# Kernel tuning notes

Hardware: AMD Instinct MI355X
Metric: run time of the kernel (lower is better)

Reference implementation:

```python
import jax, jax.numpy as jnp
import numpy as np

N, S, W, H = 256, 64, 256, 32   # node_num, sensor_num, slide_win, gru_hid_size
ALPHA = 0.2
NEG = -9e15


def gat(h, adj, Wm, a):
    """pyGAT GraphAttentionLayer (concat=False, dropout=0 / eval).
    h: [..., M, din], adj: [..., M, M], Wm: [..., din, dout], a: [..., 2*dout]."""
    Wh = jnp.einsum('...mi,...io->...mo', h, Wm)
    dout = Wm.shape[-1]
    f1 = jnp.einsum('...mo,...o->...m', Wh, a[..., :dout])
    f2 = jnp.einsum('...mo,...o->...m', Wh, a[..., dout:])
    e = jax.nn.leaky_relu(f1[..., :, None] + f2[..., None, :], negative_slope=ALPHA)
    att = jax.nn.softmax(jnp.where(adj > 0, e, NEG), axis=-1)
    return jnp.einsum('...mk,...ko->...mo', att, Wh)


def gru_cell(h, x, Wih, Whh, bih, bhh):
    # per-node batched torch GRU cell; gate order r, z, n
    gi = jnp.einsum('ngi,ni->ng', Wih, x) + bih
    gh = jnp.einsum('ngh,nh->ng', Whh, h) + bhh
    ir, iz, inn = jnp.split(gi, 3, axis=-1)
    hr, hz, hn = jnp.split(gh, 3, axis=-1)
    r = jax.nn.sigmoid(ir + hr)
    z = jax.nn.sigmoid(iz + hz)
    n = jnp.tanh(inn + r * hn)
    return (1.0 - z) * n + z * h


def gru2(xseq, h0, Wih0, Whh0, bih0, bhh0, Wih1, Whh1, bih1, bhh1):
    # xseq: [N, S, Din] (seq axis = sensor axis), h0: [2, N, H] -> ([N,S,H], [2,N,H])
    def step(carry, x_t):
        h0c, h1c = carry
        h0n = gru_cell(h0c, x_t, Wih0, Whh0, bih0, bhh0)
        h1n = gru_cell(h1c, h0n, Wih1, Whh1, bih1, bhh1)
        return (h0n, h1n), h1n
    (h0f, h1f), ys = jax.lax.scan(step, (h0[0], h0[1]), jnp.swapaxes(xseq, 0, 1))
    return jnp.swapaxes(ys, 0, 1), jnp.stack([h0f, h1f])


def setup_inputs():
    key = jax.random.key(0)
    ks = jax.random.split(key, 32)
    def rn(k, shape, scale=0.05):
        return jax.random.normal(k, shape, dtype=jnp.float32) * scale
    inp = {}
    inp['x'] = jax.random.normal(ks[0], (N, S, W), dtype=jnp.float32)
    inp['Feature_adj_sub'] = jax.random.randint(ks[1], (N, S, S), 0, 2).astype(jnp.float32)
    inp['Time_adj_sub'] = jax.random.randint(ks[2], (N, W, W), 0, 2).astype(jnp.float32)
    inp['adj'] = jax.random.randint(ks[3], (N, N), 0, 2).astype(jnp.float32)
    inp['H_pre'] = jax.random.normal(ks[4], (2, N, H), dtype=jnp.float32)
    # per-node GAT params (stacked over nodes)
    inp['Fatt_W'] = rn(ks[5], (N, W, W)); inp['Fatt_a'] = rn(ks[6], (N, 2 * W))
    inp['Tatt_W'] = rn(ks[7], (N, S, S)); inp['Tatt_a'] = rn(ks[8], (N, 2 * S))
    # per-node 2-layer GRU params
    inp['Wih0'] = rn(ks[9], (N, 3 * H, 3 * W)); inp['Whh0'] = rn(ks[10], (N, 3 * H, H))
    inp['bih0'] = rn(ks[11], (N, 3 * H)); inp['bhh0'] = rn(ks[12], (N, 3 * H))
    inp['Wih1'] = rn(ks[13], (N, 3 * H, H)); inp['Whh1'] = rn(ks[14], (N, 3 * H, H))
    inp['bih1'] = rn(ks[15], (N, 3 * H)); inp['bhh1'] = rn(ks[16], (N, 3 * H))
    # per-node 3-layer FC
    inp['fc1_w'] = rn(ks[17], (N, H, H)); inp['fc1_b'] = rn(ks[18], (N, H))
    inp['fc2_w'] = rn(ks[19], (N, H, H)); inp['fc2_b'] = rn(ks[20], (N, H))
    inp['fc3_w'] = rn(ks[21], (N, 1, H)); inp['fc3_b'] = rn(ks[22], (N, 1))
    # global output GATs
    inp['oW'] = rn(ks[23], (S, S)); inp['oa'] = rn(ks[24], (2 * S,))
    inp['o1W'] = rn(ks[25], (S, S)); inp['o1a'] = rn(ks[26], (2 * S,))
    inp['o2W'] = rn(ks[27], (2 * S, S)); inp['o2a'] = rn(ks[28], (2 * S,))
    return inp


def reference(x, Feature_adj_sub, Time_adj_sub, adj, H_pre,
              Fatt_W, Fatt_a, Tatt_W, Tatt_a,
              Wih0, Whh0, bih0, bhh0, Wih1, Whh1, bih1, bhh1,
              fc1_w, fc1_b, fc2_w, fc2_b, fc3_w, fc3_b,
              oW, oa, o1W, o1a, o2W, o2a):
    # batched over all nodes at once (replaces Python loop over node_num)
    Fat = gat(x, Feature_adj_sub, Fatt_W, Fatt_a)                    # [N,S,W]
    Tat = gat(jnp.swapaxes(x, 1, 2), Time_adj_sub, Tatt_W, Tatt_a)   # [N,W,S]
    cat_at = jnp.concatenate([Fat, jnp.swapaxes(Tat, 1, 2), x], axis=-1)  # [N,S,3W]
    gru_out, cat_H = gru2(cat_at, H_pre, Wih0, Whh0, bih0, bhh0,
                          Wih1, Whh1, bih1, bhh1)                    # [N,S,H],[2,N,H]
    h = jax.nn.relu(jnp.einsum('nsh,nkh->nsk', gru_out, fc1_w) + fc1_b[:, None, :])
    h = jax.nn.relu(jnp.einsum('nsh,nkh->nsk', h, fc2_w) + fc2_b[:, None, :])
    ct = (jnp.einsum('nsh,nkh->nsk', h, fc3_w) + fc3_b[:, None, :])[..., 0]  # [N,S]
    out = gat(ct, adj, oW, oa)
    out1 = gat(ct, adj, o1W, o1a)
    finalout = gat(jnp.concatenate([out, out1], axis=-1), adj, o2W, o2a)
    return finalout, cat_H
```

## Files before the change

### kernel.cpp

```cpp
#include <hip/hip_runtime.h>
#include <hip/hip_bf16.h>

__device__ __forceinline__ float sigf(float x){ return __builtin_amdgcn_rcpf(1.f+__expf(-x)); }
__device__ __forceinline__ float tanhfa(float x){
  return 1.f - 2.f*__builtin_amdgcn_rcpf(1.f + __expf(2.f*x));
}

#define ALPHA 0.2f
#define NEGV  -9e15f


__device__ __forceinline__ void gl2lds16(const float* g, float* l){
  __builtin_amdgcn_global_load_lds(
      (const __attribute__((address_space(1))) void*)g,
      (__attribute__((address_space(3))) void*)l, 16, 0, 0);
}

__global__ __launch_bounds__(256) void k_mask(const float* __restrict__ src,
                                              unsigned* __restrict__ dst, int nelem){
  const int stride = gridDim.x * blockDim.x;
  const int lane = threadIdx.x & 63;
  for (int e = blockIdx.x*blockDim.x + threadIdx.x; e < nelem; e += stride){
    unsigned long long m = __ballot(src[e] > 0.f);
    if (lane == 0)       dst[e >> 5] = (unsigned)m;
    else if (lane == 32) dst[e >> 5] = (unsigned)(m >> 32);
  }
}

__global__ __launch_bounds__(256) void k3_wht(const float* __restrict__ x,
                                              const float* __restrict__ TW,
                                              const float* __restrict__ Ta,
                                              float* __restrict__ WhTt,
                                              float* __restrict__ Tf1p,
                                              float* __restrict__ Tf2p){
  const int n = blockIdx.x >> 1, ch = blockIdx.x & 1, c0 = ch*32;
  const int tid = threadIdx.x;
  __shared__ float Wm[64][36];
  __shared__ float as1[32], as2[32];
  for (int idx = tid; idx < 2048; idx += 256){
    int k = idx >> 5, cc = idx & 31;
    Wm[k][cc] = TW[n*4096 + k*64 + c0 + cc];
  }
  if (tid < 32){ as1[tid] = Ta[n*128 + c0 + tid]; as2[tid] = Ta[n*128 + 64 + c0 + tid]; }
  __syncthreads();
  const int i = tid;
  const float* xn = x + n*16384;
  float acc[32];
#pragma unroll
  for (int c = 0; c < 32; ++c) acc[c] = 0.f;
#pragma unroll 2
  for (int k = 0; k < 64; ++k){
    float xv = xn[k*256 + i];
    const float* wr = &Wm[k][0];
#pragma unroll
    for (int c = 0; c < 32; ++c) acc[c] = fmaf(xv, wr[c], acc[c]);
  }
  float f1 = 0.f, f2 = 0.f;
#pragma unroll
  for (int c = 0; c < 32; ++c){ f1 = fmaf(acc[c], as1[c], f1); f2 = fmaf(acc[c], as2[c], f2); }
  Tf1p[ch*65536 + n*256 + i] = f1;
  Tf2p[ch*65536 + n*256 + i] = f2;
  float* o = WhTt + n*16384 + i*64 + c0;
#pragma unroll
  for (int q = 0; q < 8; ++q)
    *(float4*)&o[4*q] = make_float4(acc[4*q], acc[4*q+1], acc[4*q+2], acc[4*q+3]);
}

__global__ __launch_bounds__(256) void k4_tat(const float* __restrict__ WhTt,
                                              const float* __restrict__ Tf1p,
                                              const float* __restrict__ Tf2p,
                                              const unsigned* __restrict__ maskT,
                                              float* __restrict__ TatT){
  const int n = blockIdx.x >> 1, ch = blockIdx.x & 1, c0 = ch*32;
  const int tid = threadIdx.x;
  __shared__ float wtL[8192];
  __shared__ float ptb[8192];
  __shared__ float f2s[256];
  __shared__ float ssum[256];
  __shared__ float wmax[4];
  {
    const int w = tid >> 6, l = tid & 63;
    const float* src = WhTt + n*16384 + (w*64 + (l>>3))*64 + c0 + (l&7)*4;
    float* dst = &wtL[w*2048];
#pragma unroll
    for (int r = 0; r < 8; ++r) gl2lds16(src + r*512, dst + r*256);
  }
  const float f1  = Tf1p[n*256 + tid] + Tf1p[65536 + n*256 + tid];
  const float f2v = Tf2p[n*256 + tid] + Tf2p[65536 + n*256 + tid];
  f2s[tid] = f2v;
  unsigned mw[8];
#pragma unroll
  for (int w = 0; w < 8; ++w) mw[w] = maskT[n*2048 + tid*8 + w];
  float wm = f2v;
#pragma unroll
  for (int d = 1; d < 64; d <<= 1) wm = fmaxf(wm, __shfl_xor(wm, d));
  if ((tid & 63) == 0) wmax[tid >> 6] = wm;
  asm volatile("s_waitcnt vmcnt(0)" ::: "memory");
  __syncthreads();
  const float mb = fmaxf(fmaxf(wmax[0], wmax[1]), fmaxf(wmax[2], wmax[3]));
  const float tm = f1 + mb;
  const float m  = (tm > 0.f) ? tm : ALPHA*tm;
  const int iq = tid & 63, cq = tid >> 6;
  float acc[4][8];
#pragma unroll
  for (int r = 0; r < 4; ++r)
#pragma unroll
    for (int c = 0; c < 8; ++c) acc[r][c] = 0.f;
  float sloc = 0.f;
  for (int jt = 0; jt < 8; ++jt){
    const int j0 = jt*32;
#pragma unroll
    for (int jj = 0; jj < 32; jj += 4){
      const float4 f2q = *(const float4*)&f2s[j0 + jj];
      const unsigned mk = mw[(j0 + jj) >> 5];
      const int sh = (j0 + jj) & 31;
      float t0 = f1 + f2q.x; t0 = (t0 > 0.f) ? t0 : ALPHA*t0;
      float t1 = f1 + f2q.y; t1 = (t1 > 0.f) ? t1 : ALPHA*t1;
      float t2 = f1 + f2q.z; t2 = (t2 > 0.f) ? t2 : ALPHA*t2;
      float t3 = f1 + f2q.w; t3 = (t3 > 0.f) ? t3 : ALPHA*t3;
      const float e0 = ((mk >> (sh+0)) & 1u) ? __expf(t0 - m) : 0.f;
      const float e1 = ((mk >> (sh+1)) & 1u) ? __expf(t1 - m) : 0.f;
      const float e2 = ((mk >> (sh+2)) & 1u) ? __expf(t2 - m) : 0.f;
      const float e3 = ((mk >> (sh+3)) & 1u) ? __expf(t3 - m) : 0.f;
      sloc += (e0 + e1) + (e2 + e3);
      ptb[(jj+0)*256 + tid] = e0;
      ptb[(jj+1)*256 + tid] = e1;
      ptb[(jj+2)*256 + tid] = e2;
      ptb[(jj+3)*256 + tid] = e3;
    }
    __syncthreads();
#pragma unroll 4
    for (int jj = 0; jj < 32; ++jj){
      const float4 p4 = *(const float4*)&ptb[jj*256 + 4*iq];
      const float4 w0 = *(const float4*)&wtL[(j0+jj)*32 + cq*8];
      const float4 w1 = *(const float4*)&wtL[(j0+jj)*32 + cq*8 + 4];
#pragma unroll
      for (int r = 0; r < 4; ++r){
        const float pv = (r == 0) ? p4.x : (r == 1) ? p4.y : (r == 2) ? p4.z : p4.w;
        acc[r][0] = fmaf(pv, w0.x, acc[r][0]);
        acc[r][1] = fmaf(pv, w0.y, acc[r][1]);
        acc[r][2] = fmaf(pv, w0.z, acc[r][2]);
        acc[r][3] = fmaf(pv, w0.w, acc[r][3]);
        acc[r][4] = fmaf(pv, w1.x, acc[r][4]);
        acc[r][5] = fmaf(pv, w1.y, acc[r][5]);
        acc[r][6] = fmaf(pv, w1.z, acc[r][6]);
        acc[r][7] = fmaf(pv, w1.w, acc[r][7]);
      }
    }
    __syncthreads();
  }
  ssum[tid] = sloc;
  __syncthreads();
  float* o = TatT + n*16384;
#pragma unroll
  for (int r = 0; r < 4; ++r){
    const int i2 = 4*iq + r;
    const float sv = ssum[i2];
    const float inv = (sv > 0.f) ? __builtin_amdgcn_rcpf(sv) : 0.f;
#pragma unroll
    for (int cc = 0; cc < 8; ++cc)
      o[(c0 + cq*8 + cc)*256 + i2] = acc[r][cc] * inv;
  }
}

__global__ __launch_bounds__(256) void k1_whf(const float* __restrict__ x,
                                              const float* __restrict__ FW,
                                              float* __restrict__ WhF){
  const int n = blockIdx.x >> 1, ch = blockIdx.x & 1, c0 = ch*128;
  const int tid = threadIdx.x;
  __shared__ float xt[16384];
  {
    const int w = tid >> 6, l = tid & 63;
    const float* xg = x + n*16384 + w*4096 + l*4;
    float* ld = &xt[w*4096];
#pragma unroll
    for (int j = 0; j < 16; ++j) gl2lds16(xg + j*256, ld + j*256);
  }
  asm volatile("s_waitcnt vmcnt(0)" ::: "memory");
  __syncthreads();
  const int cq = tid & 31, iq = tid >> 5;
  const int cc = c0 + cq*4;
  const float* Wn = FW + (size_t)n*65536 + cc;
  const float* xrow = &xt[iq*8*256];
  float acc[8][4];
#pragma unroll
  for (int i = 0; i < 8; ++i)
#pragma unroll
    for (int c = 0; c < 4; ++c) acc[i][c] = 0.f;
#pragma unroll 2
  for (int k4 = 0; k4 < 64; ++k4){
    const float4 w0 = *(const float4*)&Wn[(4*k4+0)*256];
    const float4 w1 = *(const float4*)&Wn[(4*k4+1)*256];
    const float4 w2 = *(const float4*)&Wn[(4*k4+2)*256];
    const float4 w3 = *(const float4*)&Wn[(4*k4+3)*256];
#pragma unroll
    for (int i = 0; i < 8; ++i){
      const float4 xv = *(const float4*)&xrow[i*256 + 4*k4];
      acc[i][0] = fmaf(xv.x, w0.x, acc[i][0]); acc[i][0] = fmaf(xv.y, w1.x, acc[i][0]);
      acc[i][0] = fmaf(xv.z, w2.x, acc[i][0]); acc[i][0] = fmaf(xv.w, w3.x, acc[i][0]);
      acc[i][1] = fmaf(xv.x, w0.y, acc[i][1]); acc[i][1] = fmaf(xv.y, w1.y, acc[i][1]);
      acc[i][1] = fmaf(xv.z, w2.y, acc[i][1]); acc[i][1] = fmaf(xv.w, w3.y, acc[i][1]);
      acc[i][2] = fmaf(xv.x, w0.z, acc[i][2]); acc[i][2] = fmaf(xv.y, w1.z, acc[i][2]);
      acc[i][2] = fmaf(xv.z, w2.z, acc[i][2]); acc[i][2] = fmaf(xv.w, w3.z, acc[i][2]);
      acc[i][3] = fmaf(xv.x, w0.w, acc[i][3]); acc[i][3] = fmaf(xv.y, w1.w, acc[i][3]);
      acc[i][3] = fmaf(xv.z, w2.w, acc[i][3]); acc[i][3] = fmaf(xv.w, w3.w, acc[i][3]);
    }
  }
  float* o = WhF + n*16384 + cc;
#pragma unroll
  for (int i = 0; i < 8; ++i)
    *(float4*)&o[(iq*8 + i)*256] = make_float4(acc[i][0], acc[i][1], acc[i][2], acc[i][3]);
}

__global__ __launch_bounds__(512) void k2_fat(const float* __restrict__ WhF,
                                              const float* __restrict__ Fa,
                                              const float* __restrict__ Fadj,
                                              float* __restrict__ Fat){
  const int n = blockIdx.x, tid = threadIdx.x;
  __shared__ float attT[64][68];
  __shared__ float f1s[64], f2s[64];
  __shared__ float part[64][8][2];
  const float* Wh = WhF + n*16384;
  {
    int i = tid >> 3, q = tid & 7;
    const float* an = Fa + n*512;
    float p1 = 0.f, p2 = 0.f;
    for (int cc = 0; cc < 32; ++cc){
      int c2 = q*32 + cc;
      float w = Wh[i*256 + c2];
      p1 = fmaf(w, an[c2], p1);
      p2 = fmaf(w, an[256 + c2], p2);
    }
    part[i][q][0] = p1; part[i][q][1] = p2;
  }
  __syncthreads();
  if (tid < 64){
    float s1 = 0.f, s2 = 0.f;
#pragma unroll
    for (int q = 0; q < 8; ++q){ s1 += part[tid][q][0]; s2 += part[tid][q][1]; }
    f1s[tid] = s1; f2s[tid] = s2;
  }
  __syncthreads();
  if (tid < 64){
    const int r = tid;
    const float f1 = f1s[r];
    const float* adjr = Fadj + n*4096 + r*64;
    unsigned m0 = 0, m1 = 0;
#pragma unroll
    for (int j = 0; j < 32; ++j) if (adjr[j] > 0.f) m0 |= (1u << j);
#pragma unroll
    for (int j = 0; j < 32; ++j) if (adjr[32+j] > 0.f) m1 |= (1u << j);
    float m = -INFINITY;
#pragma unroll
    for (int j = 0; j < 64; ++j){
      float e = f1 + f2s[j]; e = (e > 0.f) ? e : ALPHA*e;
      unsigned bit = (j < 32) ? ((m0 >> j) & 1u) : ((m1 >> (j-32)) & 1u);
      e = bit ? e : NEGV;
      m = fmaxf(m, e);
    }
    float s = 0.f;
#pragma unroll
    for (int j = 0; j < 64; ++j){
      float e = f1 + f2s[j]; e = (e > 0.f) ? e : ALPHA*e;
      unsigned bit = (j < 32) ? ((m0 >> j) & 1u) : ((m1 >> (j-32)) & 1u);
      e = bit ? e : NEGV;
      s += __expf(e - m);
    }
    const float inv = 1.f / s;
#pragma unroll
    for (int j = 0; j < 64; ++j){
      float e = f1 + f2s[j]; e = (e > 0.f) ? e : ALPHA*e;
      unsigned bit = (j < 32) ? ((m0 >> j) & 1u) : ((m1 >> (j-32)) & 1u);
      e = bit ? e : NEGV;
      attT[j][r] = __expf(e - m) * inv;
    }
  }
  __syncthreads();
  const int c = tid & 255, ih = tid >> 8;
  float acc[32];
#pragma unroll
  for (int i = 0; i < 32; ++i) acc[i] = 0.f;
#pragma unroll 2
  for (int j = 0; j < 64; ++j){
    float w = Wh[j*256 + c];
    const float* ar = &attT[j][ih*32];
#pragma unroll
    for (int i = 0; i < 32; ++i) acc[i] = fmaf(ar[i], w, acc[i]);
  }
  float* o = Fat + n*16384;
#pragma unroll
  for (int i = 0; i < 32; ++i) o[(ih*32 + i)*256 + c] = acc[i];
}

__global__ __launch_bounds__(256) void k5_gi0(const float* __restrict__ Fat,
                                              const float* __restrict__ TatT,
                                              const float* __restrict__ x,
                                              const float* __restrict__ Wih0,
                                              float* __restrict__ P0,
                                              float* __restrict__ P1,
                                              float* __restrict__ P2){
  const int n = blockIdx.x & 255, s = blockIdx.x >> 8;
  const int tid = threadIdx.x;
  const int a = tid & 31, b = tid >> 5;
  __shared__ float cl[2][2304];
  const float* src = (s == 0) ? (Fat + n*16384)
                   : (s == 1) ? (TatT + n*16384)
                              : (x + n*16384);
  const float* Wseg = Wih0 + (size_t)n*73728 + s*256 + (size_t)b*12*768;
  const int tr = tid >> 2, kq = tid & 3;
  const float* cg = src + tr*256 + kq*8;
  const int cwo = tr*36 + kq*8;
  {
    float4 ra = *(const float4*)cg;
    float4 rb = *(const float4*)(cg + 4);
    *(float4*)&cl[0][cwo]     = ra;
    *(float4*)&cl[0][cwo + 4] = rb;
  }
  __syncthreads();
  float acc[12][2];
#pragma unroll
  for (int gi = 0; gi < 12; ++gi){ acc[gi][0] = 0.f; acc[gi][1] = 0.f; }
#pragma unroll 1
  for (int kt = 0; kt < 8; ++kt){
    const int buf = kt & 1;
    float4 na, nb;
    if (kt < 7){
      na = *(const float4*)(cg + (kt+1)*32);
      nb = *(const float4*)(cg + (kt+1)*32 + 4);
    }
    const float* Wk = Wseg + kt*32;
    const float* c0p = &cl[buf][a*36];
    const float* c1p = &cl[buf][(a+32)*36];
#pragma unroll
    for (int k4 = 0; k4 < 8; ++k4){
      float4 wv[12];
#pragma unroll
      for (int gi = 0; gi < 12; ++gi)
        wv[gi] = *(const float4*)(Wk + (size_t)gi*768 + k4*4);
      const float4 c0 = *(const float4*)(c0p + k4*4);
      const float4 c1 = *(const float4*)(c1p + k4*4);
#pragma unroll
      for (int gi = 0; gi < 12; ++gi){
        float a0 = acc[gi][0], a1 = acc[gi][1];
        a0 = fmaf(wv[gi].x, c0.x, a0); a1 = fmaf(wv[gi].x, c1.x, a1);
        a0 = fmaf(wv[gi].y, c0.y, a0); a1 = fmaf(wv[gi].y, c1.y, a1);
        a0 = fmaf(wv[gi].z, c0.z, a0); a1 = fmaf(wv[gi].z, c1.z, a1);
        a0 = fmaf(wv[gi].w, c0.w, a0); a1 = fmaf(wv[gi].w, c1.w, a1);
        acc[gi][0] = a0; acc[gi][1] = a1;
      }
    }
    if (kt < 7){
      *(float4*)&cl[buf^1][cwo]     = na;
      *(float4*)&cl[buf^1][cwo + 4] = nb;
    }
    __syncthreads();
  }
  float* o = (s == 0) ? (P0 + n*16384)
           : (s == 1) ? (P1 + n*16384)
                      : (P2 + n*8192);
#pragma unroll
  for (int q = 0; q < 3; ++q){
    *(float4*)&o[a*96 + b*12 + q*4] =
        make_float4(acc[4*q][0], acc[4*q+1][0], acc[4*q+2][0], acc[4*q+3][0]);
    *(float4*)&o[(a+32)*96 + b*12 + q*4] =
        make_float4(acc[4*q][1], acc[4*q+1][1], acc[4*q+2][1], acc[4*q+3][1]);
  }
}

__global__ __launch_bounds__(128) void k6_gru(const float* __restrict__ G0,
                                              const float* __restrict__ G1,
                                              const float* __restrict__ G2,
                                              const float* __restrict__ Hpre,
                                              const float* __restrict__ Whh0,
                                              const float* __restrict__ bih0,
                                              const float* __restrict__ bhh0,
                                              const float* __restrict__ Wih1,
                                              const float* __restrict__ Whh1,
                                              const float* __restrict__ bih1,
                                              const float* __restrict__ bhh1,
                                              const float* __restrict__ fc1w,
                                              const float* __restrict__ fc1b,
                                              const float* __restrict__ fc2w,
                                              const float* __restrict__ fc2b,
                                              const float* __restrict__ fc3w,
                                              const float* __restrict__ fc3b,
                                              float* __restrict__ ct,
                                              float* __restrict__ dout){
  const int n = blockIdx.x, tid = threadIdx.x;
  const int wid = tid >> 6, l = tid & 63;
  const int g2 = l & 31, co = (l >> 5) * 16;
  __shared__ float ginS[6144];
  __shared__ float h0buf[2][32];
  __shared__ float h1buf[2][32];
  __shared__ float hist[64][33];
  __shared__ float Wst[32][33];
  __shared__ float b1s[32], b2s[32], w3s[32];
  {
    const float4* p0 = (const float4*)(G0 + n*16384);
    const float4* p1 = (const float4*)(G1 + n*16384);
    const float4* p2 = (const float4*)(G2 + n*8192);
    float4* gs = (float4*)ginS;
#pragma unroll
    for (int j = 0; j < 12; ++j){
      int idx = j*128 + tid;
      float4 a = p0[idx], b = p1[idx], c = p2[idx];
      gs[idx] = make_float4(a.x+b.x+c.x, a.y+b.y+c.y, a.z+b.z+c.z, a.w+b.w+c.w);
    }
  }
  if (tid < 32){
    b1s[tid] = fc1b[n*32 + tid];
    b2s[tid] = fc2b[n*32 + tid];
    w3s[tid] = fc3w[n*32 + tid];
  }
  for (int idx = tid; idx < 1024; idx += 128) Wst[idx>>5][idx&31] = fc1w[n*1024 + idx];
  float wr_[16], wz_[16], wn_[16];
  float ur_[16], uz_[16], un_[16];
  {
    const float* WA = (wid == 0) ? (Whh0 + n*3072) : (Wih1 + n*3072);
#pragma unroll
    for (int q = 0; q < 4; ++q){
      float4 v;
      v = *(const float4*)(WA + g2*32 + co + 4*q);       wr_[4*q]=v.x; wr_[4*q+1]=v.y; wr_[4*q+2]=v.z; wr_[4*q+3]=v.w;
      v = *(const float4*)(WA + (32+g2)*32 + co + 4*q);  wz_[4*q]=v.x; wz_[4*q+1]=v.y; wz_[4*q+2]=v.z; wz_[4*q+3]=v.w;
      v = *(const float4*)(WA + (64+g2)*32 + co + 4*q);  wn_[4*q]=v.x; wn_[4*q+1]=v.y; wn_[4*q+2]=v.z; wn_[4*q+3]=v.w;
    }
    if (wid == 1){
      const float* WB = Whh1 + n*3072;
#pragma unroll
      for (int q = 0; q < 4; ++q){
        float4 v;
        v = *(const float4*)(WB + g2*32 + co + 4*q);       ur_[4*q]=v.x; ur_[4*q+1]=v.y; ur_[4*q+2]=v.z; ur_[4*q+3]=v.w;
        v = *(const float4*)(WB + (32+g2)*32 + co + 4*q);  uz_[4*q]=v.x; uz_[4*q+1]=v.y; uz_[4*q+2]=v.z; uz_[4*q+3]=v.w;
        v = *(const float4*)(WB + (64+g2)*32 + co + 4*q);  un_[4*q]=v.x; un_[4*q+1]=v.y; un_[4*q+2]=v.z; un_[4*q+3]=v.w;
      }
    }
  }
  const float* bip = (wid == 0) ? bih0 : bih1;
  const float* bhp = (wid == 0) ? bhh0 : bhh1;
  const float br = bip[n*96 + g2], bz = bip[n*96 + 32 + g2], bn = bip[n*96 + 64 + g2];
  const float cr = bhp[n*96 + g2], cz = bhp[n*96 + 32 + g2], cn = bhp[n*96 + 64 + g2];
  const float* hp = (wid == 0) ? (Hpre + n*32) : (Hpre + 8192 + n*32);
  float hown = hp[g2];
  float hs[16];
#pragma unroll
  for (int q = 0; q < 4; ++q){
    float4 v = *(const float4*)&hp[co + 4*q];
    hs[4*q]=v.x; hs[4*q+1]=v.y; hs[4*q+2]=v.z; hs[4*q+3]=v.w;
  }
  for (int s = 0; s < 65; ++s){
    __syncthreads();
    if (wid == 0){
      if (s < 64){
        const float gr = ginS[s*96 + g2], gz = ginS[s*96 + 32 + g2], gn = ginS[s*96 + 64 + g2];
        if (s > 0){
#pragma unroll
          for (int q = 0; q < 4; ++q){
            float4 v = *(const float4*)&h0buf[(s-1)&1][co + 4*q];
            hs[4*q]=v.x; hs[4*q+1]=v.y; hs[4*q+2]=v.z; hs[4*q+3]=v.w;
          }
        }
        float pr = 0.f, pz = 0.f, pn = 0.f;
#pragma unroll
        for (int j = 0; j < 16; ++j){
          pr = fmaf(wr_[j], hs[j], pr);
          pz = fmaf(wz_[j], hs[j], pz);
          pn = fmaf(wn_[j], hs[j], pn);
        }
        pr += __shfl_xor(pr, 32);
        pz += __shfl_xor(pz, 32);
        pn += __shfl_xor(pn, 32);
        const float r = sigf(gr + br + pr + cr);
        const float z = sigf(gz + bz + pz + cz);
        const float nn = tanhfa(gn + bn + r*(pn + cn));
        hown = (1.f - z)*nn + z*hown;
        if (l < 32) h0buf[s & 1][g2] = hown;
      }
    } else {
      if (s >= 1){
        const int t = s - 1;
        if (s > 1){
#pragma unroll
          for (int q = 0; q < 4; ++q){
            float4 v = *(const float4*)&h1buf[(s-1)&1][co + 4*q];
            hs[4*q]=v.x; hs[4*q+1]=v.y; hs[4*q+2]=v.z; hs[4*q+3]=v.w;
          }
        }
        float hx[16];
#pragma unroll
        for (int q = 0; q < 4; ++q){
          float4 v = *(const float4*)&h0buf[(s-1)&1][co + 4*q];
          hx[4*q]=v.x; hx[4*q+1]=v.y; hx[4*q+2]=v.z; hx[4*q+3]=v.w;
        }
        float qr = 0.f, qz = 0.f, qn = 0.f, sr = 0.f, sz = 0.f, sn = 0.f;
#pragma unroll
        for (int j = 0; j < 16; ++j){
          qr = fmaf(wr_[j], hx[j], qr);  sr = fmaf(ur_[j], hs[j], sr);
          qz = fmaf(wz_[j], hx[j], qz);  sz = fmaf(uz_[j], hs[j], sz);
          qn = fmaf(wn_[j], hx[j], qn);  sn = fmaf(un_[j], hs[j], sn);
        }
        float vr = qr + sr; vr += __shfl_xor(vr, 32);
        float vz = qz + sz; vz += __shfl_xor(vz, 32);
        qn += __shfl_xor(qn, 32);
        sn += __shfl_xor(sn, 32);
        const float r1 = sigf(vr + br + cr);
        const float z1 = sigf(vz + bz + cz);
        const float n1 = tanhfa(qn + bn + r1*(sn + cn));
        hown = (1.f - z1)*n1 + z1*hown;
        if (l < 32){ h1buf[s & 1][g2] = hown; hist[t][g2] = hown; }
      }
    }
  }
  if (wid == 0 && l < 32) dout[16384 + n*32 + g2] = hown;
  if (wid == 1 && l < 32) dout[16384 + 8192 + n*32 + g2] = hown;
  __syncthreads();
  float r1a[32];
  if (tid < 64){
    float hr[32];
#pragma unroll
    for (int k = 0; k < 32; ++k) hr[k] = hist[tid][k];
#pragma unroll
    for (int k = 0; k < 32; ++k){
      float a0=0.f,a1=0.f,a2=0.f,a3=0.f;
#pragma unroll
      for (int q = 0; q < 32; q += 4){
        a0 = fmaf(hr[q],   Wst[k][q],   a0);
        a1 = fmaf(hr[q+1], Wst[k][q+1], a1);
        a2 = fmaf(hr[q+2], Wst[k][q+2], a2);
        a3 = fmaf(hr[q+3], Wst[k][q+3], a3);
      }
      float v = b1s[k] + ((a0+a1)+(a2+a3));
      r1a[k] = v > 0.f ? v : 0.f;
    }
  }
  __syncthreads();
  for (int idx = tid; idx < 1024; idx += 128) Wst[idx>>5][idx&31] = fc2w[n*1024 + idx];
  __syncthreads();
  if (tid < 64){
    float r2a[32];
#pragma unroll
    for (int k = 0; k < 32; ++k){
      float a0=0.f,a1=0.f,a2=0.f,a3=0.f;
#pragma unroll
      for (int q = 0; q < 32; q += 4){
        a0 = fmaf(r1a[q],   Wst[k][q],   a0);
        a1 = fmaf(r1a[q+1], Wst[k][q+1], a1);
        a2 = fmaf(r1a[q+2], Wst[k][q+2], a2);
        a3 = fmaf(r1a[q+3], Wst[k][q+3], a3);
      }
      float v = b2s[k] + ((a0+a1)+(a2+a3));
      r2a[k] = v > 0.f ? v : 0.f;
    }
    float v = fc3b[n];
#pragma unroll
    for (int k = 0; k < 32; ++k) v = fmaf(r2a[k], w3s[k], v);
    ct[n*64 + tid] = v;
  }
}

__global__ __launch_bounds__(256) void k8a(const float* __restrict__ ct,
                                           const float* __restrict__ W0,
                                           const float* __restrict__ a0,
                                           const float* __restrict__ W1,
                                           const float* __restrict__ a1,
                                           float* __restrict__ WhABt,
                                           float* __restrict__ OF1,
                                           float* __restrict__ OF2){
  const int gat = blockIdx.x >> 2, rq = blockIdx.x & 3, r0 = rq*64;
  const int tid = threadIdx.x;
  const int ii = tid & 63, cq = tid >> 6;
  __shared__ float ctl[64][65];
  __shared__ float Wl[64][68];
  __shared__ float a1s[64], a2s[64];
  __shared__ float red[64][4][2];
  const float* W = gat ? W1 : W0;
  const float* aa = gat ? a1 : a0;
  for (int idx = tid; idx < 4096; idx += 256){
    int i2 = idx >> 6, k = idx & 63;
    ctl[i2][k] = ct[(r0 + i2)*64 + k];
  }
  for (int idx = tid; idx < 4096; idx += 256){
    int k = idx >> 6, c = idx & 63;
    Wl[k][c] = W[k*64 + c];
  }
  if (tid < 64){ a1s[tid] = aa[tid]; a2s[tid] = aa[64 + tid]; }
  __syncthreads();
  float acc[16];
#pragma unroll
  for (int c = 0; c < 16; ++c) acc[c] = 0.f;
#pragma unroll 2
  for (int k = 0; k < 64; ++k){
    float v = ctl[ii][k];
    const float* wr = &Wl[k][cq*16];
#pragma unroll
    for (int c = 0; c < 16; ++c) acc[c] = fmaf(v, wr[c], acc[c]);
  }
  float p1 = 0.f, p2 = 0.f;
#pragma unroll
  for (int c = 0; c < 16; ++c){
    p1 = fmaf(acc[c], a1s[cq*16 + c], p1);
    p2 = fmaf(acc[c], a2s[cq*16 + c], p2);
  }
  red[ii][cq][0] = p1; red[ii][cq][1] = p2;
  float* o = WhABt + gat*16384;
#pragma unroll
  for (int c = 0; c < 16; ++c) o[(cq*16 + c)*256 + r0 + ii] = acc[c];
  __syncthreads();
  if (cq == 0){
    OF1[gat*256 + r0 + ii] = red[ii][0][0] + red[ii][1][0] + red[ii][2][0] + red[ii][3][0];
    OF2[gat*256 + r0 + ii] = red[ii][0][1] + red[ii][1][1] + red[ii][2][1] + red[ii][3][1];
  }
}

__global__ __launch_bounds__(256) void k8b(const float* __restrict__ WhABt,
                                           const float* __restrict__ OF1,
                                           const float* __restrict__ OF2,
                                           const unsigned* __restrict__ maskA,
                                           float* __restrict__ OUTT){
  const int gat = blockIdx.x >> 2, c0 = (blockIdx.x & 3) * 16;
  const int i = threadIdx.x;
  __shared__ float wt[4096];
  __shared__ float f2s[256];
  __shared__ float wmax[4];
  {
    const int w = i >> 6, l = i & 63;
    const float* src = WhABt + gat*16384 + c0*256 + w*1024 + l*4;
    float* dst = &wt[w*1024];
#pragma unroll
    for (int r = 0; r < 4; ++r) gl2lds16(src + r*256, dst + r*256);
  }
  const float f1  = OF1[gat*256 + i];
  const float f2v = OF2[gat*256 + i];
  f2s[i] = f2v;
  unsigned mw[8];
#pragma unroll
  for (int w = 0; w < 8; ++w) mw[w] = maskA[i*8 + w];
  float wm = f2v;
#pragma unroll
  for (int d = 1; d < 64; d <<= 1) wm = fmaxf(wm, __shfl_xor(wm, d));
  if ((i & 63) == 0) wmax[i >> 6] = wm;
  asm volatile("s_waitcnt vmcnt(0)" ::: "memory");
  __syncthreads();
  const float mb = fmaxf(fmaxf(wmax[0], wmax[1]), fmaxf(wmax[2], wmax[3]));
  const float tm = f1 + mb;
  const float m  = (tm > 0.f) ? tm : ALPHA*tm;
  float acc[16];
#pragma unroll
  for (int c = 0; c < 16; ++c) acc[c] = 0.f;
  float s = 0.f;
#pragma unroll 2
  for (int jb = 0; jb < 64; ++jb){
    const float4 f2q = *(const float4*)&f2s[jb*4];
    const unsigned mk = mw[jb >> 3];
    const int sh = (jb & 7) * 4;
    float t0 = f1 + f2q.x; t0 = (t0 > 0.f) ? t0 : ALPHA*t0;
    float t1 = f1 + f2q.y; t1 = (t1 > 0.f) ? t1 : ALPHA*t1;
    float t2 = f1 + f2q.z; t2 = (t2 > 0.f) ? t2 : ALPHA*t2;
    float t3 = f1 + f2q.w; t3 = (t3 > 0.f) ? t3 : ALPHA*t3;
    const float e0 = ((mk >> (sh+0)) & 1u) ? __expf(t0 - m) : 0.f;
    const float e1 = ((mk >> (sh+1)) & 1u) ? __expf(t1 - m) : 0.f;
    const float e2 = ((mk >> (sh+2)) & 1u) ? __expf(t2 - m) : 0.f;
    const float e3 = ((mk >> (sh+3)) & 1u) ? __expf(t3 - m) : 0.f;
    s += (e0 + e1) + (e2 + e3);
#pragma unroll
    for (int c = 0; c < 16; ++c){
      const float4 wv = *(const float4*)&wt[c*256 + jb*4];
      acc[c] = fmaf(e0, wv.x, fmaf(e1, wv.y, fmaf(e2, wv.z, fmaf(e3, wv.w, acc[c]))));
    }
  }
  const float inv = (s > 0.f) ? __builtin_amdgcn_rcpf(s) : 0.f;
#pragma unroll
  for (int c = 0; c < 16; ++c) OUTT[gat*16384 + (c0+c)*256 + i] = acc[c] * inv;
}

__global__ __launch_bounds__(256) void k8c(const float* __restrict__ OUTT,
                                           const float* __restrict__ W2,
                                           const float* __restrict__ a2,
                                           float* __restrict__ Wh2,
                                           float* __restrict__ F1B,
                                           float* __restrict__ F2B){
  const int r0 = blockIdx.x * 32;
  const int tid = threadIdx.x;
  const int ii = tid & 31, cq = tid >> 5;
  __shared__ float W2l[128][68];
  __shared__ float a1s[64], a2s[64];
  __shared__ float red[32][8][2];
  for (int idx = tid; idx < 8192; idx += 256){
    int k = idx >> 6, c = idx & 63;
    W2l[k][c] = W2[k*64 + c];
  }
  if (tid < 64){ a1s[tid] = a2[tid]; a2s[tid] = a2[64 + tid]; }
  __syncthreads();
  float acc[8];
#pragma unroll
  for (int c = 0; c < 8; ++c) acc[c] = 0.f;
#pragma unroll 2
  for (int k = 0; k < 128; ++k){
    float v = OUTT[(k >> 6)*16384 + (k & 63)*256 + r0 + ii];
    const float* wr = &W2l[k][cq*8];
#pragma unroll
    for (int c = 0; c < 8; ++c) acc[c] = fmaf(v, wr[c], acc[c]);
  }
  float p1 = 0.f, p2 = 0.f;
#pragma unroll
  for (int c = 0; c < 8; ++c){
    p1 = fmaf(acc[c], a1s[cq*8 + c], p1);
    p2 = fmaf(acc[c], a2s[cq*8 + c], p2);
  }
  red[ii][cq][0] = p1; red[ii][cq][1] = p2;
#pragma unroll
  for (int c = 0; c < 8; ++c) Wh2[(cq*8 + c)*256 + r0 + ii] = acc[c];
  __syncthreads();
  if (cq == 0){
    float s1 = 0.f, s2 = 0.f;
#pragma unroll
    for (int q = 0; q < 8; ++q){ s1 += red[ii][q][0]; s2 += red[ii][q][1]; }
    F1B[r0 + ii] = s1; F2B[r0 + ii] = s2;
  }
}

__global__ __launch_bounds__(256) void k8d(const float* __restrict__ Wh2,
                                           const float* __restrict__ F1B,
                                           const float* __restrict__ F2B,
                                           const unsigned* __restrict__ maskA,
                                           float* __restrict__ dOut){
  const int c0 = blockIdx.x * 16;
  const int i = threadIdx.x;
  __shared__ float wt[4096];
  __shared__ float f2s[256];
  __shared__ float wmax[4];
  {
    const int w = i >> 6, l = i & 63;
    const float* src = Wh2 + c0*256 + w*1024 + l*4;
    float* dst = &wt[w*1024];
#pragma unroll
    for (int r = 0; r < 4; ++r) gl2lds16(src + r*256, dst + r*256);
  }
  const float f1  = F1B[i];
  const float f2v = F2B[i];
  f2s[i] = f2v;
  unsigned mw[8];
#pragma unroll
  for (int w = 0; w < 8; ++w) mw[w] = maskA[i*8 + w];
  float wm = f2v;
#pragma unroll
  for (int d = 1; d < 64; d <<= 1) wm = fmaxf(wm, __shfl_xor(wm, d));
  if ((i & 63) == 0) wmax[i >> 6] = wm;
  asm volatile("s_waitcnt vmcnt(0)" ::: "memory");
  __syncthreads();
  const float mb = fmaxf(fmaxf(wmax[0], wmax[1]), fmaxf(wmax[2], wmax[3]));
  const float tm = f1 + mb;
  const float m  = (tm > 0.f) ? tm : ALPHA*tm;
  float acc[16];
#pragma unroll
  for (int c = 0; c < 16; ++c) acc[c] = 0.f;
  float s = 0.f;
#pragma unroll 2
  for (int jb = 0; jb < 64; ++jb){
    const float4 f2q = *(const float4*)&f2s[jb*4];
    const unsigned mk = mw[jb >> 3];
    const int sh = (jb & 7) * 4;
    float t0 = f1 + f2q.x; t0 = (t0 > 0.f) ? t0 : ALPHA*t0;
    float t1 = f1 + f2q.y; t1 = (t1 > 0.f) ? t1 : ALPHA*t1;
    float t2 = f1 + f2q.z; t2 = (t2 > 0.f) ? t2 : ALPHA*t2;
    float t3 = f1 + f2q.w; t3 = (t3 > 0.f) ? t3 : ALPHA*t3;
    const float e0 = ((mk >> (sh+0)) & 1u) ? __expf(t0 - m) : 0.f;
    const float e1 = ((mk >> (sh+1)) & 1u) ? __expf(t1 - m) : 0.f;
    const float e2 = ((mk >> (sh+2)) & 1u) ? __expf(t2 - m) : 0.f;
    const float e3 = ((mk >> (sh+3)) & 1u) ? __expf(t3 - m) : 0.f;
    s += (e0 + e1) + (e2 + e3);
#pragma unroll
    for (int c = 0; c < 16; ++c){
      const float4 wv = *(const float4*)&wt[c*256 + jb*4];
      acc[c] = fmaf(e0, wv.x, fmaf(e1, wv.y, fmaf(e2, wv.z, fmaf(e3, wv.w, acc[c]))));
    }
  }
  const float inv = (s > 0.f) ? __builtin_amdgcn_rcpf(s) : 0.f;
#pragma unroll
  for (int c = 0; c < 16; ++c) dOut[i*64 + c0 + c] = acc[c] * inv;
}

extern "C" void kernel_launch(void* const* d_in, const int* in_sizes, int n_in,
                              void* d_out, int out_size, void* d_ws, size_t ws_size,
                              hipStream_t stream){
  (void)in_sizes; (void)n_in; (void)out_size; (void)ws_size;
  const float* x     = (const float*)d_in[0];
  const float* Fadj  = (const float*)d_in[1];
  const float* Tadj  = (const float*)d_in[2];
  const float* adj   = (const float*)d_in[3];
  const float* Hpre  = (const float*)d_in[4];
  const float* FattW = (const float*)d_in[5];
  const float* Fatta = (const float*)d_in[6];
  const float* TattW = (const float*)d_in[7];
  const float* Tatta = (const float*)d_in[8];
  const float* Wih0  = (const float*)d_in[9];
  const float* Whh0  = (const float*)d_in[10];
  const float* bih0  = (const float*)d_in[11];
  const float* bhh0  = (const float*)d_in[12];
  const float* Wih1  = (const float*)d_in[13];
  const float* Whh1  = (const float*)d_in[14];
  const float* bih1  = (const float*)d_in[15];
  const float* bhh1  = (const float*)d_in[16];
  const float* fc1w  = (const float*)d_in[17];
  const float* fc1b  = (const float*)d_in[18];
  const float* fc2w  = (const float*)d_in[19];
  const float* fc2b  = (const float*)d_in[20];
  const float* fc3w  = (const float*)d_in[21];
  const float* fc3b  = (const float*)d_in[22];
  const float* oW    = (const float*)d_in[23];
  const float* oa    = (const float*)d_in[24];
  const float* o1W   = (const float*)d_in[25];
  const float* o1a   = (const float*)d_in[26];
  const float* o2W   = (const float*)d_in[27];
  const float* o2a   = (const float*)d_in[28];
  float* out = (float*)d_out;

  float* ws = (float*)d_ws;
  float* R0 = ws;
  float* R1 = ws + 4194304;
  float* R2 = ws + 8388608;
  unsigned* maskT = (unsigned*)R2;
  float* Tf1p = R2 + 524288;
  float* Tf2p = R2 + 655360;
  unsigned* maskA = (unsigned*)(ws + 12582912);
  float* WhTt = R0;
  float* WhF  = R0;
  float* TatT = R1;
  float* Fat  = R2;
  float* P0 = R2;
  float* P1 = R1;
  float* P2 = R0;
  float* ctb   = R0 + 2097152;
  float* WhABt = R1 + 16384;
  float* OF1   = R1 + 49152;
  float* OF2   = R1 + 49664;
  float* OUTT  = R1 + 50176;
  float* WH2   = R1 + 82944;
  float* F1B   = R1 + 99328;
  float* F2B   = R1 + 99584;

  k_mask<<<1024, 256, 0, stream>>>(Tadj, maskT, 16777216);
  k_mask<<<32, 256, 0, stream>>>(adj, maskA, 65536);
  k3_wht<<<512, 256, 0, stream>>>(x, TattW, Tatta, WhTt, Tf1p, Tf2p);
  k4_tat<<<512, 256, 0, stream>>>(WhTt, Tf1p, Tf2p, maskT, TatT);
  k1_whf<<<512, 256, 0, stream>>>(x, FattW, WhF);
  k2_fat<<<256, 512, 0, stream>>>(WhF, Fatta, Fadj, Fat);
  k5_gi0<<<768, 256, 0, stream>>>(Fat, TatT, x, Wih0, P0, P1, P2);
  k6_gru<<<256, 128, 0, stream>>>(P0, P1, P2, Hpre, Whh0, bih0, bhh0, Wih1, Whh1, bih1, bhh1,
                                  fc1w, fc1b, fc2w, fc2b, fc3w, fc3b, ctb, out);
  k8a<<<8, 256, 0, stream>>>(ctb, oW, oa, o1W, o1a, WhABt, OF1, OF2);
  k8b<<<8, 256, 0, stream>>>(WhABt, OF1, OF2, maskA, OUTT);
  k8c<<<8, 256, 0, stream>>>(OUTT, o2W, o2a, WH2, F1B, F2B);
  k8d<<<4, 256, 0, stream>>>(WH2, F1B, F2B, maskA, out);
}
```

Baseline: 655.7 us.

## Stage Wih0 tiles in LDS and enlarge per-thread register tile in gi0 GEMM

The input-gate projection kernel now double-buffers both the Wih0 weight slice and the activation slice through shared memory, instead of reading weights straight from global memory per thread. Each thread computes a 12x4 output tile instead of 12x2, and the block size halves to 128 threads. This aims to cut redundant global/L2 weight traffic and raise FMA-to-load ratio, at the cost of more LDS (about 46 KB), more registers and fewer threads per block, which may lower occupancy.

```diff
diff --git a/kernel.cpp b/kernel.cpp
--- a/kernel.cpp
+++ b/kernel.cpp
@@ -292,66 +292,101 @@
   for (int i = 0; i < 32; ++i) o[(ih*32 + i)*256 + c] = acc[i];
 }
 
-__global__ __launch_bounds__(256) void k5_gi0(const float* __restrict__ Fat,
-                                              const float* __restrict__ TatT,
-                                              const float* __restrict__ x,
-                                              const float* __restrict__ Wih0,
-                                              float* __restrict__ P0,
-                                              float* __restrict__ P1,
-                                              float* __restrict__ P2){
+__global__ __launch_bounds__(128, 1) void k5_gi0(const float* __restrict__ Fat,
+                                                 const float* __restrict__ TatT,
+                                                 const float* __restrict__ x,
+                                                 const float* __restrict__ Wih0,
+                                                 float* __restrict__ P0,
+                                                 float* __restrict__ P1,
+                                                 float* __restrict__ P2){
   const int n = blockIdx.x & 255, s = blockIdx.x >> 8;
   const int tid = threadIdx.x;
-  const int a = tid & 31, b = tid >> 5;
+  const int b = tid >> 4, ta = tid & 15;
+  __shared__ float wl[2][3456];
   __shared__ float cl[2][2304];
   const float* src = (s == 0) ? (Fat + n*16384)
                    : (s == 1) ? (TatT + n*16384)
                               : (x + n*16384);
-  const float* Wseg = Wih0 + (size_t)n*73728 + s*256 + (size_t)b*12*768;
-  const int tr = tid >> 2, kq = tid & 3;
-  const float* cg = src + tr*256 + kq*8;
-  const int cwo = tr*36 + kq*8;
-  {
-    float4 ra = *(const float4*)cg;
-    float4 rb = *(const float4*)(cg + 4);
-    *(float4*)&cl[0][cwo]     = ra;
-    *(float4*)&cl[0][cwo + 4] = rb;
-  }
-  __syncthreads();
-  float acc[12][2];
-#pragma unroll
-  for (int gi = 0; gi < 12; ++gi){ acc[gi][0] = 0.f; acc[gi][1] = 0.f; }
+  const float* Wseg = Wih0 + (size_t)n*73728 + s*256;
+  float4 wreg[6], creg[4];
+#pragma unroll
+  for (int j = 0; j < 6; ++j){
+    const int qid = j*128 + tid, row = qid >> 3, q = qid & 7;
+    wreg[j] = *(const float4*)(Wseg + (size_t)row*768 + q*4);
+  }
+#pragma unroll
+  for (int j = 0; j < 4; ++j){
+    const int qid = j*128 + tid, row = qid >> 3, q = qid & 7;
+    creg[j] = *(const float4*)(src + row*256 + q*4);
+  }
+#pragma unroll
+  for (int j = 0; j < 6; ++j){
+    const int qid = j*128 + tid, row = qid >> 3, q = qid & 7;
+    *(float4*)&wl[0][row*36 + q*4] = wreg[j];
+  }
+#pragma unroll
+  for (int j = 0; j < 4; ++j){
+    const int qid = j*128 + tid, row = qid >> 3, q = qid & 7;
+    *(float4*)&cl[0][row*36 + q*4] = creg[j];
+  }
+  __syncthreads();
+  float acc[12][4];
+#pragma unroll
+  for (int gi = 0; gi < 12; ++gi)
+#pragma unroll
+    for (int r = 0; r < 4; ++r) acc[gi][r] = 0.f;
 #pragma unroll 1
   for (int kt = 0; kt < 8; ++kt){
     const int buf = kt & 1;
-    float4 na, nb;
     if (kt < 7){
-      na = *(const float4*)(cg + (kt+1)*32);
-      nb = *(const float4*)(cg + (kt+1)*32 + 4);
-    }
-    const float* Wk = Wseg + kt*32;
-    const float* c0p = &cl[buf][a*36];
-    const float* c1p = &cl[buf][(a+32)*36];
+#pragma unroll
+      for (int j = 0; j < 6; ++j){
+        const int qid = j*128 + tid, row = qid >> 3, q = qid & 7;
+        wreg[j] = *(const float4*)(Wseg + (size_t)row*768 + (kt+1)*32 + q*4);
+      }
+#pragma unroll
+      for (int j = 0; j < 4; ++j){
+        const int qid = j*128 + tid, row = qid >> 3, q = qid & 7;
+        creg[j] = *(const float4*)(src + row*256 + (kt+1)*32 + q*4);
+      }
+    }
+    const float* wb = &wl[buf][b*432];
+    const float* cb = &cl[buf][ta*144];
 #pragma unroll
     for (int k4 = 0; k4 < 8; ++k4){
       float4 wv[12];
 #pragma unroll
       for (int gi = 0; gi < 12; ++gi)
-        wv[gi] = *(const float4*)(Wk + (size_t)gi*768 + k4*4);
-      const float4 c0 = *(const float4*)(c0p + k4*4);
-      const float4 c1 = *(const float4*)(c1p + k4*4);
+        wv[gi] = *(const float4*)(wb + gi*36 + k4*4);
+      const float4 c0 = *(const float4*)(cb + 0*36 + k4*4);
+      const float4 c1 = *(const float4*)(cb + 1*36 + k4*4);
+      const float4 c2 = *(const float4*)(cb + 2*36 + k4*4);
+      const float4 c3 = *(const float4*)(cb + 3*36 + k4*4);
 #pragma unroll
       for (int gi = 0; gi < 12; ++gi){
-        float a0 = acc[gi][0], a1 = acc[gi][1];
+        float a0 = acc[gi][0], a1 = acc[gi][1], a2 = acc[gi][2], a3 = acc[gi][3];
         a0 = fmaf(wv[gi].x, c0.x, a0); a1 = fmaf(wv[gi].x, c1.x, a1);
+        a2 = fmaf(wv[gi].x, c2.x, a2); a3 = fmaf(wv[gi].x, c3.x, a3);
         a0 = fmaf(wv[gi].y, c0.y, a0); a1 = fmaf(wv[gi].y, c1.y, a1);
+        a2 = fmaf(wv[gi].y, c2.y, a2); a3 = fmaf(wv[gi].y, c3.y, a3);
         a0 = fmaf(wv[gi].z, c0.z, a0); a1 = fmaf(wv[gi].z, c1.z, a1);
+        a2 = fmaf(wv[gi].z, c2.z, a2); a3 = fmaf(wv[gi].z, c3.z, a3);
         a0 = fmaf(wv[gi].w, c0.w, a0); a1 = fmaf(wv[gi].w, c1.w, a1);
-        acc[gi][0] = a0; acc[gi][1] = a1;
+        a2 = fmaf(wv[gi].w, c2.w, a2); a3 = fmaf(wv[gi].w, c3.w, a3);
+        acc[gi][0] = a0; acc[gi][1] = a1; acc[gi][2] = a2; acc[gi][3] = a3;
       }
     }
     if (kt < 7){
-      *(float4*)&cl[buf^1][cwo]     = na;
-      *(float4*)&cl[buf^1][cwo + 4] = nb;
+#pragma unroll
+      for (int j = 0; j < 6; ++j){
+        const int qid = j*128 + tid, row = qid >> 3, q = qid & 7;
+        *(float4*)&wl[buf^1][row*36 + q*4] = wreg[j];
+      }
+#pragma unroll
+      for (int j = 0; j < 4; ++j){
+        const int qid = j*128 + tid, row = qid >> 3, q = qid & 7;
+        *(float4*)&cl[buf^1][row*36 + q*4] = creg[j];
+      }
     }
     __syncthreads();
   }
@@ -359,11 +394,12 @@
            : (s == 1) ? (P1 + n*16384)
                       : (P2 + n*8192);
 #pragma unroll
-  for (int q = 0; q < 3; ++q){
-    *(float4*)&o[a*96 + b*12 + q*4] =
-        make_float4(acc[4*q][0], acc[4*q+1][0], acc[4*q+2][0], acc[4*q+3][0]);
-    *(float4*)&o[(a+32)*96 + b*12 + q*4] =
-        make_float4(acc[4*q][1], acc[4*q+1][1], acc[4*q+2][1], acc[4*q+3][1]);
+  for (int r = 0; r < 4; ++r){
+    const int t = ta*4 + r;
+#pragma unroll
+    for (int q = 0; q < 3; ++q)
+      *(float4*)&o[t*96 + b*12 + q*4] =
+          make_float4(acc[4*q][r], acc[4*q+1][r], acc[4*q+2][r], acc[4*q+3][r]);
   }
 }
 
@@ -844,7 +880,7 @@
   k4_tat<<<512, 256, 0, stream>>>(WhTt, Tf1p, Tf2p, maskT, TatT);
   k1_whf<<<512, 256, 0, stream>>>(x, FattW, WhF);
   k2_fat<<<256, 512, 0, stream>>>(WhF, Fatta, Fadj, Fat);
-  k5_gi0<<<768, 256, 0, stream>>>(Fat, TatT, x, Wih0, P0, P1, P2);
+  k5_gi0<<<768, 128, 0, stream>>>(Fat, TatT, x, Wih0, P0, P1, P2);
   k6_gru<<<256, 128, 0, stream>>>(P0, P1, P2, Hpre, Whh0, bih0, bhh0, Wih1, Whh1, bih1, bhh1,
                                   fc1w, fc1b, fc2w, fc2b, fc3w, fc3b, ctb, out);
   k8a<<<8, 256, 0, stream>>>(ctb, oW, oa, o1W, o1a, WhABt, OF1, OF2);
```

Result: slower. 779.7 us (+18.9%).
